# Kernel optimization log

Measured on AMD Instinct MI355X. Metric: run time of the kernel, lower is better.

## Reference

```python
import jax, jax.numpy as jnp
import numpy as np

N_A = 500000
N_B = 500000
NUM_HERBS = 25000
D = 128  # hidden_dim


def setup_inputs() -> dict:
    key = jax.random.key(0)
    ks = jax.random.split(key, 12)
    h_A = jax.random.normal(ks[0], (N_A, D), dtype=jnp.float32)
    h_B = jax.random.normal(ks[1], (N_B, D), dtype=jnp.float32)
    herb_idx_A = jnp.sort(jax.random.randint(ks[2], (N_A,), 0, NUM_HERBS, dtype=jnp.int64))
    herb_idx_B = jnp.sort(jax.random.randint(ks[3], (N_B,), 0, NUM_HERBS, dtype=jnp.int64))
    # attn_net: Linear(2D, D//2) -> LeakyReLU(0.2) -> Linear(D//2, 1)
    aw1 = jax.random.normal(ks[4], (2 * D, D // 2), dtype=jnp.float32) / np.sqrt(2 * D)
    ab1 = jnp.zeros((D // 2,), dtype=jnp.float32)
    aw2 = jax.random.normal(ks[5], (D // 2, 1), dtype=jnp.float32) / np.sqrt(D // 2)
    ab2 = jnp.zeros((1,), dtype=jnp.float32)
    # fusion_mlp: Linear(4D, 2D) -> ReLU -> Linear(2D, D)
    fw1 = jax.random.normal(ks[6], (4 * D, 2 * D), dtype=jnp.float32) / np.sqrt(4 * D)
    fb1 = jnp.zeros((2 * D,), dtype=jnp.float32)
    fw2 = jax.random.normal(ks[7], (2 * D, D), dtype=jnp.float32) / np.sqrt(2 * D)
    fb2 = jnp.zeros((D,), dtype=jnp.float32)
    return {"h_A": h_A, "h_B": h_B, "herb_idx_A": herb_idx_A, "herb_idx_B": herb_idx_B,
            "num_herbs": NUM_HERBS,
            "aw1": aw1, "ab1": ab1, "aw2": aw2, "ab2": ab2,
            "fw1": fw1, "fb1": fb1, "fw2": fw2, "fb2": fb2}


def _seg_mean(x, idx, n):
    s = jax.ops.segment_sum(x, idx, num_segments=n)          # [n, D]
    cnt = jax.ops.segment_sum(jnp.ones((x.shape[0], 1), x.dtype), idx, num_segments=n)
    return s / jnp.maximum(cnt, 1.0)


def _seg_softmax(score, idx, n):
    # score: [N, 1]; numerically-stable per-segment softmax (as in PyG softmax)
    m = jax.ops.segment_max(score, idx, num_segments=n)       # [n, 1]
    e = jnp.exp(score - m[idx])
    denom = jax.ops.segment_sum(e, idx, num_segments=n)
    return e / (denom[idx] + 1e-16)


def _attn(x, aw1, ab1, aw2, ab2):
    h = jax.nn.leaky_relu(x @ aw1 + ab1, negative_slope=0.2)
    return h @ aw2 + ab2                                      # [N, 1]


def reference(h_A, h_B, herb_idx_A, herb_idx_B, num_herbs,
              aw1, ab1, aw2, ab2, fw1, fb1, fw2, fb2):
    H_B_mean = _seg_mean(h_B, herb_idx_B, num_herbs)          # [H, D]
    H_A_mean = _seg_mean(h_A, herb_idx_A, num_herbs)          # [H, D]

    cat_A = jnp.concatenate([h_A, H_B_mean[herb_idx_A]], axis=-1)  # [N_A, 2D]
    alpha_A = _seg_softmax(_attn(cat_A, aw1, ab1, aw2, ab2), herb_idx_A, num_herbs)
    H_A_given_B = jax.ops.segment_sum(alpha_A * h_A, herb_idx_A, num_segments=num_herbs)

    cat_B = jnp.concatenate([h_B, H_A_mean[herb_idx_B]], axis=-1)  # [N_B, 2D]
    alpha_B = _seg_softmax(_attn(cat_B, aw1, ab1, aw2, ab2), herb_idx_B, num_herbs)
    H_B_given_A = jax.ops.segment_sum(alpha_B * h_B, herb_idx_B, num_segments=num_herbs)

    concat_feat = jnp.concatenate([H_A_given_B, H_B_given_A,
                                   H_A_given_B * H_B_given_A,
                                   jnp.abs(H_A_given_B - H_B_given_A)], axis=-1)  # [H, 4D]
    H_interaction = jax.nn.relu(concat_feat @ fw1 + fb1) @ fw2 + fb2              # [H, D]
    return (H_interaction, H_A_given_B, H_B_given_A)
```

## Files before the change

kernel.cpp:

```cpp
#include <hip/hip_runtime.h>
#include <math.h>

#define H_HERBS 25000
#define DIM 128

typedef __attribute__((ext_vector_type(8))) short bf16x8;
typedef __attribute__((ext_vector_type(4))) float f32x4;

__device__ inline unsigned pack2bf(float a, float b) {
    union { float f; unsigned u; } x, y; x.f = a; y.f = b;
    return ((x.u + 0x8000u) >> 16) | ((y.u + 0x8000u) & 0xFFFF0000u);
}

__global__ void k_starts(const int* __restrict__ idxA, const int* __restrict__ idxB,
                         int nA, int nB, int* __restrict__ startA, int* __restrict__ startB) {
    int h = blockIdx.x * blockDim.x + threadIdx.x;
    if (h > H_HERBS) return;
    {
        int lo = 0, hi = nA;
        while (lo < hi) { int mid = (lo + hi) >> 1; if (idxA[mid] < h) lo = mid + 1; else hi = mid; }
        startA[h] = lo;
    }
    {
        int lo = 0, hi = nB;
        while (lo < hi) { int mid = (lo + hi) >> 1; if (idxB[mid] < h) lo = mid + 1; else hi = mid; }
        startB[h] = lo;
    }
}

__global__ __launch_bounds__(64) void k_packw(
        const float* __restrict__ fw1, const float* __restrict__ fw2,
        uint4* __restrict__ w1bf, uint4* __restrict__ w2bf) {
    int b = blockIdx.x, l = threadIdx.x;
    int c = l & 15, kg = l >> 4;
    if (b < 256) {
        int kt = b >> 4, nt = b & 15;
        int k0 = kt * 32 + kg * 8, j = nt * 16 + c;
        unsigned u0 = pack2bf(fw1[(size_t)(k0 + 0) * 256 + j], fw1[(size_t)(k0 + 1) * 256 + j]);
        unsigned u1 = pack2bf(fw1[(size_t)(k0 + 2) * 256 + j], fw1[(size_t)(k0 + 3) * 256 + j]);
        unsigned u2 = pack2bf(fw1[(size_t)(k0 + 4) * 256 + j], fw1[(size_t)(k0 + 5) * 256 + j]);
        unsigned u3 = pack2bf(fw1[(size_t)(k0 + 6) * 256 + j], fw1[(size_t)(k0 + 7) * 256 + j]);
        w1bf[(size_t)b * 64 + l] = make_uint4(u0, u1, u2, u3);
    } else {
        int bb = b - 256;
        int kt = bb >> 3, nt = bb & 7;
        int k0 = kt * 32 + kg * 8, j = nt * 16 + c;
        unsigned u0 = pack2bf(fw2[(size_t)(k0 + 0) * 128 + j], fw2[(size_t)(k0 + 1) * 128 + j]);
        unsigned u1 = pack2bf(fw2[(size_t)(k0 + 2) * 128 + j], fw2[(size_t)(k0 + 3) * 128 + j]);
        unsigned u2 = pack2bf(fw2[(size_t)(k0 + 4) * 128 + j], fw2[(size_t)(k0 + 5) * 128 + j]);
        unsigned u3 = pack2bf(fw2[(size_t)(k0 + 6) * 128 + j], fw2[(size_t)(k0 + 7) * 128 + j]);
        w2bf[(size_t)bb * 64 + l] = make_uint4(u0, u1, u2, u3);
    }
}

__global__ __launch_bounds__(256) void k_mean_proj(
        const float* __restrict__ X, const int* __restrict__ start,
        const float* __restrict__ aw1, const float* __restrict__ ab1,
        float* __restrict__ mpart) {
    __shared__ __align__(16) float mb[16][128];
    int h0 = blockIdx.x * 16;
    int t = threadIdx.x;

    int wv = t >> 6, ln = t & 63, half = ln >> 5, li = ln & 31;
    const float4* X4 = (const float4*)X;
    #pragma unroll
    for (int i = 0; i < 4; ++i) {
        int hh = wv * 4 + i;
        int h = h0 + hh;
        if (h >= H_HERBS) { if (half == 0) ((float4*)mb[hh])[li] = make_float4(0.f,0.f,0.f,0.f); continue; }
        int s = start[h], e = start[h + 1];
        float4 acc = make_float4(0.f, 0.f, 0.f, 0.f);
        int r = s + half;
        for (; r + 6 < e; r += 8) {
            float4 v0 = X4[(size_t)r * 32 + li];
            float4 v1 = X4[(size_t)(r + 2) * 32 + li];
            float4 v2 = X4[(size_t)(r + 4) * 32 + li];
            float4 v3 = X4[(size_t)(r + 6) * 32 + li];
            acc.x += (v0.x + v1.x) + (v2.x + v3.x);
            acc.y += (v0.y + v1.y) + (v2.y + v3.y);
            acc.z += (v0.z + v1.z) + (v2.z + v3.z);
            acc.w += (v0.w + v1.w) + (v2.w + v3.w);
        }
        for (; r < e; r += 2) {
            float4 v0 = X4[(size_t)r * 32 + li];
            acc.x += v0.x; acc.y += v0.y; acc.z += v0.z; acc.w += v0.w;
        }
        acc.x += __shfl_xor(acc.x, 32, 64);
        acc.y += __shfl_xor(acc.y, 32, 64);
        acc.z += __shfl_xor(acc.z, 32, 64);
        acc.w += __shfl_xor(acc.w, 32, 64);
        int cnt = e - s;
        float inv = 1.0f / (float)(cnt > 1 ? cnt : 1);
        if (half == 0) {
            ((float4*)mb[hh])[li] = make_float4(acc.x * inv, acc.y * inv, acc.z * inv, acc.w * inv);
        }
    }
    __syncthreads();

    {
        int j = t & 63, wg = t >> 6;
        const float* Wg = aw1 + 128 * 64;
        float b1 = ab1[j];
        float a0 = b1, a1 = b1, a2 = b1, a3 = b1;
        #pragma unroll 8
        for (int k = 0; k < 128; ++k) {
            float w = Wg[k * 64 + j];
            a0 += mb[wg * 4 + 0][k] * w;
            a1 += mb[wg * 4 + 1][k] * w;
            a2 += mb[wg * 4 + 2][k] * w;
            a3 += mb[wg * 4 + 3][k] * w;
        }
        int h = h0 + wg * 4;
        if (h + 0 < H_HERBS) mpart[(size_t)(h + 0) * 64 + j] = a0;
        if (h + 1 < H_HERBS) mpart[(size_t)(h + 1) * 64 + j] = a1;
        if (h + 2 < H_HERBS) mpart[(size_t)(h + 2) * 64 + j] = a2;
        if (h + 3 < H_HERBS) mpart[(size_t)(h + 3) * 64 + j] = a3;
    }
}

__global__ __launch_bounds__(256) void k_mpart_one(
        const float* __restrict__ meanG, const float* __restrict__ aw1,
        const float* __restrict__ ab1, float* __restrict__ mpart) {
    __shared__ float Wl[128 * 64];
    __shared__ float mb[64 * 128];
    int h0 = blockIdx.x * 64;
    int t = threadIdx.x;

    const float4* Wsrc = (const float4*)(aw1 + 128 * 64);
    float4* Wl4 = (float4*)Wl;
    #pragma unroll
    for (int q = 0; q < 8; ++q) Wl4[t + 256 * q] = Wsrc[t + 256 * q];
    float4* mb4 = (float4*)mb;
    const float4* mG4 = (const float4*)meanG;
    #pragma unroll
    for (int q = 0; q < 8; ++q) {
        int ent = t + 256 * q;
        int hl = ent >> 5, kq = ent & 31;
        int h = h0 + hl;
        mb4[ent] = (h < H_HERBS) ? mG4[(size_t)h * 32 + kq] : make_float4(0.f, 0.f, 0.f, 0.f);
    }
    __syncthreads();

    int j = t & 63, hg = t >> 6;
    float b1 = ab1[j];
    #pragma unroll
    for (int ii = 0; ii < 4; ++ii) {
        int hl0 = hg * 16 + ii * 4;
        float a0 = 0.f, a1 = 0.f, a2 = 0.f, a3 = 0.f;
        for (int k = 0; k < 128; ++k) {
            float w = Wl[k * 64 + j];
            a0 += mb[(hl0 + 0) * 128 + k] * w;
            a1 += mb[(hl0 + 1) * 128 + k] * w;
            a2 += mb[(hl0 + 2) * 128 + k] * w;
            a3 += mb[(hl0 + 3) * 128 + k] * w;
        }
        int h = h0 + hl0;
        if (h + 0 < H_HERBS) mpart[(size_t)(h + 0) * 64 + j] = b1 + a0;
        if (h + 1 < H_HERBS) mpart[(size_t)(h + 1) * 64 + j] = b1 + a1;
        if (h + 2 < H_HERBS) mpart[(size_t)(h + 2) * 64 + j] = b1 + a2;
        if (h + 3 < H_HERBS) mpart[(size_t)(h + 3) * 64 + j] = b1 + a3;
    }
}

__global__ __launch_bounds__(256) void k_scores_one(
        const float* __restrict__ X, const int* __restrict__ idx,
        const float* __restrict__ mpart,
        const float* __restrict__ aw1, const float* __restrict__ aw2,
        const float* __restrict__ ab2,
        float* __restrict__ scores, int n) {
    int t = threadIdx.x;
    int l = t & 63, wid = t >> 6;
    int c = l & 15, kg = l >> 4;

    union ABu { bf16x8 v; unsigned u[4]; };

    ABu wf[4][4];
    #pragma unroll
    for (int kb = 0; kb < 4; ++kb) {
        int k0 = kb * 32 + kg * 8;
        #pragma unroll
        for (int nb = 0; nb < 4; ++nb) {
            int j = nb * 16 + c;
            #pragma unroll
            for (int e = 0; e < 4; ++e) {
                wf[kb][nb].u[e] = pack2bf(aw1[(size_t)(k0 + 2 * e)     * 64 + j],
                                          aw1[(size_t)(k0 + 2 * e + 1) * 64 + j]);
            }
        }
    }
    float a2[4];
    #pragma unroll
    for (int nb = 0; nb < 4; ++nb) a2[nb] = aw2[nb * 16 + c];
    float b2s = ab2[0];

    for (int pass = 0; pass < 4; ++pass) {
        long r0 = (long)blockIdx.x * 256 + pass * 64 + wid * 16;
        if (r0 >= n) break;
        long myrow = r0 + c;
        if (myrow >= n) myrow = n - 1;
        const float4* Xr = (const float4*)(X + (size_t)myrow * DIM);

        ABu af[4];
        #pragma unroll
        for (int kb = 0; kb < 4; ++kb) {
            float4 a = Xr[kb * 8 + kg * 2];
            float4 b = Xr[kb * 8 + kg * 2 + 1];
            af[kb].u[0] = pack2bf(a.x, a.y);
            af[kb].u[1] = pack2bf(a.z, a.w);
            af[kb].u[2] = pack2bf(b.x, b.y);
            af[kb].u[3] = pack2bf(b.z, b.w);
        }

        f32x4 acc[4];
        #pragma unroll
        for (int nb = 0; nb < 4; ++nb) { acc[nb].x = 0.f; acc[nb].y = 0.f; acc[nb].z = 0.f; acc[nb].w = 0.f; }
        #pragma unroll
        for (int kb = 0; kb < 4; ++kb) {
            #pragma unroll
            for (int nb = 0; nb < 4; ++nb) {
                acc[nb] = __builtin_amdgcn_mfma_f32_16x16x32_bf16(af[kb].v, wf[kb][nb].v, acc[nb], 0, 0, 0);
            }
        }

        int rgrp = kg * 4;
        float part[4] = {0.f, 0.f, 0.f, 0.f};
        #pragma unroll
        for (int reg = 0; reg < 4; ++reg) {
            long rr = r0 + rgrp + reg;
            bool v = rr < n;
            int h = v ? idx[rr] : 0;
            const float* mp = mpart + (size_t)h * 64;
            #pragma unroll
            for (int nb = 0; nb < 4; ++nb) {
                float hv = acc[nb][reg] + mp[nb * 16 + c];
                hv = hv > 0.f ? hv : 0.2f * hv;
                part[reg] += hv * a2[nb];
            }
        }
        #pragma unroll
        for (int reg = 0; reg < 4; ++reg) {
            float p = part[reg];
            p += __shfl_xor(p, 1, 64);
            p += __shfl_xor(p, 2, 64);
            p += __shfl_xor(p, 4, 64);
            p += __shfl_xor(p, 8, 64);
            part[reg] = p;
        }
        if (c == 0) {
            #pragma unroll
            for (int reg = 0; reg < 4; ++reg) {
                long rr = r0 + rgrp + reg;
                if (rr < n) scores[rr] = part[reg] + b2s;
            }
        }
    }
}

template <bool WITH_MEAN>
__global__ __launch_bounds__(64) void k_attn_one(
        const float* __restrict__ X, const int* __restrict__ start,
        const float* __restrict__ scores,
        float* __restrict__ out, float* __restrict__ meanOut) {
    int h = blockIdx.x;
    int lane = threadIdx.x;
    int half = lane >> 5, li = lane & 31;
    int s = start[h], e = start[h + 1];
    const float4* X4 = (const float4*)X;
    float4 acc = make_float4(0.f, 0.f, 0.f, 0.f);
    float4 accS = make_float4(0.f, 0.f, 0.f, 0.f);
    if (e > s) {
        float mx = -INFINITY;
        for (int r = s + lane; r < e; r += 64) mx = fmaxf(mx, scores[r]);
        #pragma unroll
        for (int o = 32; o; o >>= 1) mx = fmaxf(mx, __shfl_xor(mx, o, 64));
        float sum = 0.f;
        for (int r = s + lane; r < e; r += 64) sum += __expf(scores[r] - mx);
        #pragma unroll
        for (int o = 32; o; o >>= 1) sum += __shfl_xor(sum, o, 64);
        float invden = 1.0f / (sum + 1e-16f);

        int r = s + half;
        for (; r + 6 < e; r += 8) {
            float w0 = __expf(scores[r]     - mx) * invden;
            float w1 = __expf(scores[r + 2] - mx) * invden;
            float w2 = __expf(scores[r + 4] - mx) * invden;
            float w3 = __expf(scores[r + 6] - mx) * invden;
            float4 v0 = X4[(size_t)r * 32 + li];
            float4 v1 = X4[(size_t)(r + 2) * 32 + li];
            float4 v2 = X4[(size_t)(r + 4) * 32 + li];
            float4 v3 = X4[(size_t)(r + 6) * 32 + li];
            acc.x += (w0 * v0.x + w1 * v1.x) + (w2 * v2.x + w3 * v3.x);
            acc.y += (w0 * v0.y + w1 * v1.y) + (w2 * v2.y + w3 * v3.y);
            acc.z += (w0 * v0.z + w1 * v1.z) + (w2 * v2.z + w3 * v3.z);
            acc.w += (w0 * v0.w + w1 * v1.w) + (w2 * v2.w + w3 * v3.w);
            if (WITH_MEAN) {
                accS.x += (v0.x + v1.x) + (v2.x + v3.x);
                accS.y += (v0.y + v1.y) + (v2.y + v3.y);
                accS.z += (v0.z + v1.z) + (v2.z + v3.z);
                accS.w += (v0.w + v1.w) + (v2.w + v3.w);
            }
        }
        for (; r < e; r += 2) {
            float w0 = __expf(scores[r] - mx) * invden;
            float4 v0 = X4[(size_t)r * 32 + li];
            acc.x += w0 * v0.x; acc.y += w0 * v0.y;
            acc.z += w0 * v0.z; acc.w += w0 * v0.w;
            if (WITH_MEAN) {
                accS.x += v0.x; accS.y += v0.y; accS.z += v0.z; accS.w += v0.w;
            }
        }
    }
    acc.x += __shfl_xor(acc.x, 32, 64);
    acc.y += __shfl_xor(acc.y, 32, 64);
    acc.z += __shfl_xor(acc.z, 32, 64);
    acc.w += __shfl_xor(acc.w, 32, 64);
    if (WITH_MEAN) {
        accS.x += __shfl_xor(accS.x, 32, 64);
        accS.y += __shfl_xor(accS.y, 32, 64);
        accS.z += __shfl_xor(accS.z, 32, 64);
        accS.w += __shfl_xor(accS.w, 32, 64);
    }
    if (half == 0) {
        ((float4*)out)[(size_t)h * 32 + li] = acc;
        if (WITH_MEAN) {
            int cnt = e - s;
            float inv = 1.0f / (float)(cnt > 1 ? cnt : 1);
            ((float4*)meanOut)[(size_t)h * 32 + li] =
                make_float4(accS.x * inv, accS.y * inv, accS.z * inv, accS.w * inv);
        }
    }
}

__global__ __launch_bounds__(256) void k_fusion_mfma(
        const float* __restrict__ HA, const float* __restrict__ HB,
        const uint4* __restrict__ w1bf, const uint4* __restrict__ w2bf,
        const float* __restrict__ fb1, const float* __restrict__ fb2,
        float* __restrict__ out) {
    __shared__ float hid[32 * 256];
    int t = threadIdx.x, wid = t >> 6, l = t & 63, c = l & 15, kg = l >> 4;
    int h0 = blockIdx.x * 32;
    int ms = wid & 1, nh = wid >> 1;

    union ABu { bf16x8 v; unsigned u[4]; uint4 q; };

    {
        int rowl = ms * 16 + c;
        int h = h0 + rowl;
        bool hv = h < H_HERBS;
        const float* pa = HA + (size_t)(hv ? h : h0) * DIM;
        const float* pb = HB + (size_t)(hv ? h : h0) * DIM;

        f32x4 acc[8];
        #pragma unroll
        for (int nt = 0; nt < 8; ++nt) { acc[nt].x = 0.f; acc[nt].y = 0.f; acc[nt].z = 0.f; acc[nt].w = 0.f; }

        #pragma unroll
        for (int kt = 0; kt < 16; ++kt) {
            int k0 = kt * 32 + kg * 8;
            int range = k0 >> 7, off = k0 & 127;
            float f[8];
            if (range == 0) {
                float4 a0 = *(const float4*)(pa + off), a1 = *(const float4*)(pa + off + 4);
                f[0] = a0.x; f[1] = a0.y; f[2] = a0.z; f[3] = a0.w;
                f[4] = a1.x; f[5] = a1.y; f[6] = a1.z; f[7] = a1.w;
            } else if (range == 1) {
                float4 b0 = *(const float4*)(pb + off), b1 = *(const float4*)(pb + off + 4);
                f[0] = b0.x; f[1] = b0.y; f[2] = b0.z; f[3] = b0.w;
                f[4] = b1.x; f[5] = b1.y; f[6] = b1.z; f[7] = b1.w;
            } else if (range == 2) {
                float4 a0 = *(const float4*)(pa + off), a1 = *(const float4*)(pa + off + 4);
                float4 b0 = *(const float4*)(pb + off), b1 = *(const float4*)(pb + off + 4);
                f[0] = a0.x * b0.x; f[1] = a0.y * b0.y; f[2] = a0.z * b0.z; f[3] = a0.w * b0.w;
                f[4] = a1.x * b1.x; f[5] = a1.y * b1.y; f[6] = a1.z * b1.z; f[7] = a1.w * b1.w;
            } else {
                float4 a0 = *(const float4*)(pa + off), a1 = *(const float4*)(pa + off + 4);
                float4 b0 = *(const float4*)(pb + off), b1 = *(const float4*)(pb + off + 4);
                f[0] = fabsf(a0.x - b0.x); f[1] = fabsf(a0.y - b0.y);
                f[2] = fabsf(a0.z - b0.z); f[3] = fabsf(a0.w - b0.w);
                f[4] = fabsf(a1.x - b1.x); f[5] = fabsf(a1.y - b1.y);
                f[6] = fabsf(a1.z - b1.z); f[7] = fabsf(a1.w - b1.w);
            }
            ABu af;
            af.u[0] = pack2bf(f[0], f[1]); af.u[1] = pack2bf(f[2], f[3]);
            af.u[2] = pack2bf(f[4], f[5]); af.u[3] = pack2bf(f[6], f[7]);
            #pragma unroll
            for (int nt = 0; nt < 8; ++nt) {
                ABu bfr; bfr.q = w1bf[(size_t)(kt * 16 + nh * 8 + nt) * 64 + l];
                acc[nt] = __builtin_amdgcn_mfma_f32_16x16x32_bf16(af.v, bfr.v, acc[nt], 0, 0, 0);
            }
        }

        #pragma unroll
        for (int nt = 0; nt < 8; ++nt) {
            int j = nh * 128 + nt * 16 + c;
            float b1 = fb1[j];
            #pragma unroll
            for (int reg = 0; reg < 4; ++reg) {
                int row = ms * 16 + kg * 4 + reg;
                float v = fmaxf(acc[nt][reg] + b1, 0.f);
                hid[row * 256 + (j ^ ((row & 7) << 3))] = v;
            }
        }
    }
    __syncthreads();

    {
        int rowl = ms * 16 + c;
        f32x4 acc2[4];
        #pragma unroll
        for (int nt = 0; nt < 4; ++nt) { acc2[nt].x = 0.f; acc2[nt].y = 0.f; acc2[nt].z = 0.f; acc2[nt].w = 0.f; }

        #pragma unroll
        for (int kt = 0; kt < 8; ++kt) {
            int j0 = kt * 32 + kg * 8;
            int widx = rowl * 256 + (j0 ^ ((rowl & 7) << 3));
            float4 h0v = *(const float4*)&hid[widx];
            float4 h1v = *(const float4*)&hid[widx + 4];
            ABu af;
            af.u[0] = pack2bf(h0v.x, h0v.y); af.u[1] = pack2bf(h0v.z, h0v.w);
            af.u[2] = pack2bf(h1v.x, h1v.y); af.u[3] = pack2bf(h1v.z, h1v.w);
            #pragma unroll
            for (int nt = 0; nt < 4; ++nt) {
                ABu bfr; bfr.q = w2bf[(size_t)(kt * 8 + nh * 4 + nt) * 64 + l];
                acc2[nt] = __builtin_amdgcn_mfma_f32_16x16x32_bf16(af.v, bfr.v, acc2[nt], 0, 0, 0);
            }
        }

        #pragma unroll
        for (int nt = 0; nt < 4; ++nt) {
            int j = nh * 64 + nt * 16 + c;
            float b2 = fb2[j];
            #pragma unroll
            for (int reg = 0; reg < 4; ++reg) {
                int row = ms * 16 + kg * 4 + reg;
                int h = h0 + row;
                if (h < H_HERBS) out[(size_t)h * DIM + j] = acc2[nt][reg] + b2;
            }
        }
    }
}

extern "C" void kernel_launch(void* const* d_in, const int* in_sizes, int n_in,
                              void* d_out, int out_size, void* d_ws, size_t ws_size,
                              hipStream_t stream) {
    const float* hA  = (const float*)d_in[0];
    const float* hB  = (const float*)d_in[1];
    const int*   idxA = (const int*)d_in[2];
    const int*   idxB = (const int*)d_in[3];
    const float* aw1 = (const float*)d_in[5];
    const float* ab1 = (const float*)d_in[6];
    const float* aw2 = (const float*)d_in[7];
    const float* ab2 = (const float*)d_in[8];
    const float* fw1 = (const float*)d_in[9];
    const float* fb1 = (const float*)d_in[10];
    const float* fw2 = (const float*)d_in[11];
    const float* fb2 = (const float*)d_in[12];

    int nA = in_sizes[0] / DIM;
    int nB = in_sizes[1] / DIM;

    float* out  = (float*)d_out;
    float* outI = out;
    float* outA = out + (size_t)H_HERBS * DIM;
    float* outB = out + (size_t)2 * H_HERBS * DIM;
    float* meanA = outI;

    char* w = (char*)d_ws;
    auto carve = [&](size_t bytes) { char* p = w; w += (bytes + 255) & ~(size_t)255; return p; };
    int*   startA  = (int*)carve((size_t)(H_HERBS + 1) * sizeof(int));
    int*   startB  = (int*)carve((size_t)(H_HERBS + 1) * sizeof(int));
    float* mpartA  = (float*)carve((size_t)H_HERBS * 64 * sizeof(float));
    float* mpartB  = (float*)carve((size_t)H_HERBS * 64 * sizeof(float));
    float* scoresA = (float*)carve((size_t)nA * sizeof(float));
    float* scoresB = (float*)carve((size_t)nB * sizeof(float));
    uint4* w1bf    = (uint4*)carve((size_t)256 * 64 * sizeof(uint4));
    uint4* w2bf    = (uint4*)carve((size_t)64 * 64 * sizeof(uint4));

    int gridA = (nA + 255) / 256;
    int gridB = (nB + 255) / 256;
    int nhb16 = (H_HERBS + 15) / 16;
    int nhb64 = (H_HERBS + 63) / 64;

    k_starts<<<(H_HERBS + 1 + 255) / 256, 256, 0, stream>>>(idxA, idxB, nA, nB, startA, startB);
    k_packw<<<320, 64, 0, stream>>>(fw1, fw2, w1bf, w2bf);

    k_mean_proj<<<nhb16, 256, 0, stream>>>(hB, startB, aw1, ab1, mpartA);
    k_scores_one<<<gridA, 256, 0, stream>>>(hA, idxA, mpartA, aw1, aw2, ab2, scoresA, nA);
    k_attn_one<true><<<H_HERBS, 64, 0, stream>>>(hA, startA, scoresA, outA, meanA);
    k_mpart_one<<<nhb64, 256, 0, stream>>>(meanA, aw1, ab1, mpartB);
    k_scores_one<<<gridB, 256, 0, stream>>>(hB, idxB, mpartB, aw1, aw2, ab2, scoresB, nB);
    k_attn_one<false><<<H_HERBS, 64, 0, stream>>>(hB, startB, scoresB, outB, nullptr);
    k_fusion_mfma<<<(H_HERBS + 31) / 32, 256, 0, stream>>>(outA, outB, w1bf, w2bf, fb1, fb2, outI);
}
```

Measured before the change: 385.6 us.

## Compute segment max via atomics in score kernel and fuse softmax denominator

The score kernel now records each segment's maximum score with an order-preserving integer encoding and atomicMax. The attention kernel reads that max directly instead of running its own max pass. It also accumulates the exp-sum in the same pass as the weighted feature sum and normalises at the end, which removes two separate passes over the scores. The cost is 500k global atomics per side, with heavy contention on sorted segments of about 20 rows each. The reads being removed are small, so the gain is limited.

Result: no change. 391.3 us (+1.5%).

```diff
diff --git a/kernel.cpp b/kernel.cpp
--- a/kernel.cpp
+++ b/kernel.cpp
@@ -3,6 +3,7 @@
 
 #define H_HERBS 25000
 #define DIM 128
+#define ENC_NEG_INF 0x007FFFFFu
 
 typedef __attribute__((ext_vector_type(8))) short bf16x8;
 typedef __attribute__((ext_vector_type(4))) float f32x4;
@@ -12,8 +13,17 @@
     return ((x.u + 0x8000u) >> 16) | ((y.u + 0x8000u) & 0xFFFF0000u);
 }
 
+__device__ inline unsigned encf(float f) {
+    unsigned u = __float_as_uint(f);
+    return (u & 0x80000000u) ? ~u : (u | 0x80000000u);
+}
+__device__ inline float decf(unsigned k) {
+    return (k & 0x80000000u) ? __uint_as_float(k ^ 0x80000000u) : __uint_as_float(~k);
+}
+
 __global__ void k_starts(const int* __restrict__ idxA, const int* __restrict__ idxB,
-                         int nA, int nB, int* __restrict__ startA, int* __restrict__ startB) {
+                         int nA, int nB, int* __restrict__ startA, int* __restrict__ startB,
+                         unsigned* __restrict__ smaxA, unsigned* __restrict__ smaxB) {
     int h = blockIdx.x * blockDim.x + threadIdx.x;
     if (h > H_HERBS) return;
     {
@@ -26,6 +36,7 @@
         while (lo < hi) { int mid = (lo + hi) >> 1; if (idxB[mid] < h) lo = mid + 1; else hi = mid; }
         startB[h] = lo;
     }
+    if (h < H_HERBS) { smaxA[h] = ENC_NEG_INF; smaxB[h] = ENC_NEG_INF; }
 }
 
 __global__ __launch_bounds__(64) void k_packw(
@@ -167,7 +178,7 @@
         const float* __restrict__ mpart,
         const float* __restrict__ aw1, const float* __restrict__ aw2,
         const float* __restrict__ ab2,
-        float* __restrict__ scores, int n) {
+        float* __restrict__ scores, unsigned* __restrict__ smax, int n) {
     int t = threadIdx.x;
     int l = t & 63, wid = t >> 6;
     int c = l & 15, kg = l >> 4;
@@ -223,19 +234,23 @@
         }
 
         int rgrp = kg * 4;
-        float part[4] = {0.f, 0.f, 0.f, 0.f};
+        float part[4];
+        int hsv[4];
         #pragma unroll
         for (int reg = 0; reg < 4; ++reg) {
             long rr = r0 + rgrp + reg;
             bool v = rr < n;
             int h = v ? idx[rr] : 0;
+            hsv[reg] = h;
             const float* mp = mpart + (size_t)h * 64;
+            float p = 0.f;
             #pragma unroll
             for (int nb = 0; nb < 4; ++nb) {
                 float hv = acc[nb][reg] + mp[nb * 16 + c];
                 hv = hv > 0.f ? hv : 0.2f * hv;
-                part[reg] += hv * a2[nb];
-            }
+                p += hv * a2[nb];
+            }
+            part[reg] = p;
         }
         #pragma unroll
         for (int reg = 0; reg < 4; ++reg) {
@@ -250,7 +265,11 @@
             #pragma unroll
             for (int reg = 0; reg < 4; ++reg) {
                 long rr = r0 + rgrp + reg;
-                if (rr < n) scores[rr] = part[reg] + b2s;
+                if (rr < n) {
+                    float sval = part[reg] + b2s;
+                    scores[rr] = sval;
+                    atomicMax(&smax[hsv[reg]], encf(sval));
+                }
             }
         }
     }
@@ -259,7 +278,7 @@
 template <bool WITH_MEAN>
 __global__ __launch_bounds__(64) void k_attn_one(
         const float* __restrict__ X, const int* __restrict__ start,
-        const float* __restrict__ scores,
+        const float* __restrict__ scores, const unsigned* __restrict__ smax,
         float* __restrict__ out, float* __restrict__ meanOut) {
     int h = blockIdx.x;
     int lane = threadIdx.x;
@@ -268,31 +287,24 @@
     const float4* X4 = (const float4*)X;
     float4 acc = make_float4(0.f, 0.f, 0.f, 0.f);
     float4 accS = make_float4(0.f, 0.f, 0.f, 0.f);
+    float sumE = 0.f;
     if (e > s) {
-        float mx = -INFINITY;
-        for (int r = s + lane; r < e; r += 64) mx = fmaxf(mx, scores[r]);
-        #pragma unroll
-        for (int o = 32; o; o >>= 1) mx = fmaxf(mx, __shfl_xor(mx, o, 64));
-        float sum = 0.f;
-        for (int r = s + lane; r < e; r += 64) sum += __expf(scores[r] - mx);
-        #pragma unroll
-        for (int o = 32; o; o >>= 1) sum += __shfl_xor(sum, o, 64);
-        float invden = 1.0f / (sum + 1e-16f);
-
+        float mx = decf(smax[h]);
         int r = s + half;
         for (; r + 6 < e; r += 8) {
-            float w0 = __expf(scores[r]     - mx) * invden;
-            float w1 = __expf(scores[r + 2] - mx) * invden;
-            float w2 = __expf(scores[r + 4] - mx) * invden;
-            float w3 = __expf(scores[r + 6] - mx) * invden;
+            float e0 = __expf(scores[r]     - mx);
+            float e1 = __expf(scores[r + 2] - mx);
+            float e2 = __expf(scores[r + 4] - mx);
+            float e3 = __expf(scores[r + 6] - mx);
             float4 v0 = X4[(size_t)r * 32 + li];
             float4 v1 = X4[(size_t)(r + 2) * 32 + li];
             float4 v2 = X4[(size_t)(r + 4) * 32 + li];
             float4 v3 = X4[(size_t)(r + 6) * 32 + li];
-            acc.x += (w0 * v0.x + w1 * v1.x) + (w2 * v2.x + w3 * v3.x);
-            acc.y += (w0 * v0.y + w1 * v1.y) + (w2 * v2.y + w3 * v3.y);
-            acc.z += (w0 * v0.z + w1 * v1.z) + (w2 * v2.z + w3 * v3.z);
-            acc.w += (w0 * v0.w + w1 * v1.w) + (w2 * v2.w + w3 * v3.w);
+            sumE += (e0 + e1) + (e2 + e3);
+            acc.x += (e0 * v0.x + e1 * v1.x) + (e2 * v2.x + e3 * v3.x);
+            acc.y += (e0 * v0.y + e1 * v1.y) + (e2 * v2.y + e3 * v3.y);
+            acc.z += (e0 * v0.z + e1 * v1.z) + (e2 * v2.z + e3 * v3.z);
+            acc.w += (e0 * v0.w + e1 * v1.w) + (e2 * v2.w + e3 * v3.w);
             if (WITH_MEAN) {
                 accS.x += (v0.x + v1.x) + (v2.x + v3.x);
                 accS.y += (v0.y + v1.y) + (v2.y + v3.y);
@@ -301,10 +313,11 @@
             }
         }
         for (; r < e; r += 2) {
-            float w0 = __expf(scores[r] - mx) * invden;
+            float e0 = __expf(scores[r] - mx);
             float4 v0 = X4[(size_t)r * 32 + li];
-            acc.x += w0 * v0.x; acc.y += w0 * v0.y;
-            acc.z += w0 * v0.z; acc.w += w0 * v0.w;
+            sumE += e0;
+            acc.x += e0 * v0.x; acc.y += e0 * v0.y;
+            acc.z += e0 * v0.z; acc.w += e0 * v0.w;
             if (WITH_MEAN) {
                 accS.x += v0.x; accS.y += v0.y; accS.z += v0.z; accS.w += v0.w;
             }
@@ -314,6 +327,7 @@
     acc.y += __shfl_xor(acc.y, 32, 64);
     acc.z += __shfl_xor(acc.z, 32, 64);
     acc.w += __shfl_xor(acc.w, 32, 64);
+    sumE  += __shfl_xor(sumE, 32, 64);
     if (WITH_MEAN) {
         accS.x += __shfl_xor(accS.x, 32, 64);
         accS.y += __shfl_xor(accS.y, 32, 64);
@@ -321,7 +335,9 @@
         accS.w += __shfl_xor(accS.w, 32, 64);
     }
     if (half == 0) {
-        ((float4*)out)[(size_t)h * 32 + li] = acc;
+        float invden = 1.0f / (sumE + 1e-16f);
+        ((float4*)out)[(size_t)h * 32 + li] =
+            make_float4(acc.x * invden, acc.y * invden, acc.z * invden, acc.w * invden);
         if (WITH_MEAN) {
             int cnt = e - s;
             float inv = 1.0f / (float)(cnt > 1 ? cnt : 1);
@@ -467,28 +483,31 @@
 
     char* w = (char*)d_ws;
     auto carve = [&](size_t bytes) { char* p = w; w += (bytes + 255) & ~(size_t)255; return p; };
-    int*   startA  = (int*)carve((size_t)(H_HERBS + 1) * sizeof(int));
-    int*   startB  = (int*)carve((size_t)(H_HERBS + 1) * sizeof(int));
-    float* mpartA  = (float*)carve((size_t)H_HERBS * 64 * sizeof(float));
-    float* mpartB  = (float*)carve((size_t)H_HERBS * 64 * sizeof(float));
-    float* scoresA = (float*)carve((size_t)nA * sizeof(float));
-    float* scoresB = (float*)carve((size_t)nB * sizeof(float));
-    uint4* w1bf    = (uint4*)carve((size_t)256 * 64 * sizeof(uint4));
-    uint4* w2bf    = (uint4*)carve((size_t)64 * 64 * sizeof(uint4));
+    int*      startA  = (int*)carve((size_t)(H_HERBS + 1) * sizeof(int));
+    int*      startB  = (int*)carve((size_t)(H_HERBS + 1) * sizeof(int));
+    unsigned* smaxA   = (unsigned*)carve((size_t)H_HERBS * sizeof(unsigned));
+    unsigned* smaxB   = (unsigned*)carve((size_t)H_HERBS * sizeof(unsigned));
+    float*    mpartA  = (float*)carve((size_t)H_HERBS * 64 * sizeof(float));
+    float*    mpartB  = (float*)carve((size_t)H_HERBS * 64 * sizeof(float));
+    float*    scoresA = (float*)carve((size_t)nA * sizeof(float));
+    float*    scoresB = (float*)carve((size_t)nB * sizeof(float));
+    uint4*    w1bf    = (uint4*)carve((size_t)256 * 64 * sizeof(uint4));
+    uint4*    w2bf    = (uint4*)carve((size_t)64 * 64 * sizeof(uint4));
 
     int gridA = (nA + 255) / 256;
     int gridB = (nB + 255) / 256;
     int nhb16 = (H_HERBS + 15) / 16;
     int nhb64 = (H_HERBS + 63) / 64;
 
-    k_starts<<<(H_HERBS + 1 + 255) / 256, 256, 0, stream>>>(idxA, idxB, nA, nB, startA, startB);
+    k_starts<<<(H_HERBS + 1 + 255) / 256, 256, 0, stream>>>(idxA, idxB, nA, nB,
+                                                            startA, startB, smaxA, smaxB);
     k_packw<<<320, 64, 0, stream>>>(fw1, fw2, w1bf, w2bf);
 
     k_mean_proj<<<nhb16, 256, 0, stream>>>(hB, startB, aw1, ab1, mpartA);
-    k_scores_one<<<gridA, 256, 0, stream>>>(hA, idxA, mpartA, aw1, aw2, ab2, scoresA, nA);
-    k_attn_one<true><<<H_HERBS, 64, 0, stream>>>(hA, startA, scoresA, outA, meanA);
+    k_scores_one<<<gridA, 256, 0, stream>>>(hA, idxA, mpartA, aw1, aw2, ab2, scoresA, smaxA, nA);
+    k_attn_one<true><<<H_HERBS, 64, 0, stream>>>(hA, startA, scoresA, smaxA, outA, meanA);
     k_mpart_one<<<nhb64, 256, 0, stream>>>(meanA, aw1, ab1, mpartB);
-    k_scores_one<<<gridB, 256, 0, stream>>>(hB, idxB, mpartB, aw1, aw2, ab2, scoresB, nB);
-    k_attn_one<false><<<H_HERBS, 64, 0, stream>>>(hB, startB, scoresB, outB, nullptr);
+    k_scores_one<<<gridB, 256, 0, stream>>>(hB, idxB, mpartB, aw1, aw2, ab2, scoresB, smaxB, nB);
+    k_attn_one<false><<<H_HERBS, 64, 0, stream>>>(hB, startB, scoresB, smaxB, outB, nullptr);
     k_fusion_mfma<<<(H_HERBS + 31) / 32, 256, 0, stream>>>(outA, outB, w1bf, w2bf, fb1, fb2, outI);
 }
```
